# Kernel optimization log

Measured on AMD Instinct MI355X. Metric: run time of the kernel, lower is better.

Reference implementation:

```python
import jax, jax.numpy as jnp
import numpy as np

OBJ_N, D_KEY, D_VAL, BANK_N, N_Q, BS = 4, 128, 512, 7200, 3600, 1


def setup_inputs() -> dict:
    key = jax.random.key(0)
    k1, k2, k3, k4, k5 = jax.random.split(key, 5)
    return {
        "keys": jax.random.normal(k1, (OBJ_N, D_KEY, BANK_N), dtype=jnp.float32),
        "values": jax.random.normal(k2, (OBJ_N, D_VAL, BANK_N), dtype=jnp.float32),
        "masks": jax.random.uniform(k3, (OBJ_N, 1, BANK_N), dtype=jnp.float32),
        "q_in": jax.random.normal(k4, (BS, D_KEY, N_Q), dtype=jnp.float32),
        "q_out": jax.random.normal(k5, (BS, D_VAL, N_Q), dtype=jnp.float32),
    }


def reference(keys, values, masks, q_in, q_out):
    # keys: (O, Dk, B) memory keys per object; q_in: (S, Dk, N) query keys
    d_key = keys.shape[1]
    scale = 1.0 / jnp.sqrt(jnp.asarray(d_key, dtype=keys.dtype))
    # p[o,s,b,n] = softmax_b( keys[o,:,b] . q_in[s,:,n] / sqrt(Dk) )
    logits = jnp.einsum('odb,sdn->osbn', keys, q_in) * scale
    p = jax.nn.softmax(logits, axis=2)
    # mem[o,s,v,n] = sum_b values[o,v,b] * p[o,s,b,n]
    mem = jnp.einsum('ovb,osbn->osvn', values, p)
    # mask_mem[o,s,1,n]: mask-weighted attention readout, gates q_out
    mask_mem = jnp.einsum('omb,osbn->osmn', masks, p)
    q_out_with_mask = q_out[None] * mask_mem          # (O, S, Dv, N)
    out = jnp.concatenate([mem, q_out_with_mask], axis=2)  # (O, S, 2*Dv, N)
    return jnp.transpose(out, (1, 0, 2, 3))           # (S, O, 2*Dv, N)
```

## Files before the change

kernel.cpp:

```cpp
#include <hip/hip_runtime.h>
#include <hip/hip_bf16.h>

typedef unsigned short u16;
typedef unsigned int   u32;
typedef short bf16x8 __attribute__((ext_vector_type(8)));
typedef float f32x4  __attribute__((ext_vector_type(4)));

#define O_N    4
#define D_K    128
#define D_V    512
#define BANK   7200
#define NQ     3600
#define NT     64
#define NTILES 57
#define NSUB   225
#define VH_ROWS 256

#define P_OFF    0
#define LST_OFF  16384
#define MST_OFF  17408
#define SMEM_BYTES 18432
#define Q_OFF    0

#define MFMA16(a, b, c) __builtin_amdgcn_mfma_f32_16x16x32_bf16((a), (b), (c), 0, 0, 0)

static __device__ __forceinline__ u16 f2bf(float x) {
    u32 u = __builtin_bit_cast(u32, x);
    return (u16)((u + 0x7FFFu + ((u >> 16) & 1u)) >> 16);
}

#define QSCALE 0.12751743f


__global__ void k_transpose_bf16(const float* __restrict__ in, u16* __restrict__ out) {
    __shared__ float tile[32][33];
    const int obj = blockIdx.z;
    const float* src = in + (size_t)obj * D_K * BANK;
    u16* dst = out + (size_t)obj * BANK * D_K;
    const int bx = blockIdx.x * 32;
    const int by = blockIdx.y * 32;
    const int tx = threadIdx.x, ty = threadIdx.y;
#pragma unroll
    for (int i = 0; i < 4; i++)
        tile[ty + 8 * i][tx] = src[(size_t)(by + ty + 8 * i) * BANK + bx + tx];
    __syncthreads();
#pragma unroll
    for (int i = 0; i < 4; i++)
        dst[(size_t)(bx + ty + 8 * i) * D_K + by + tx] = f2bf(tile[tx][ty + 8 * i]);
}

__global__ void k_convert_bf16(const float* __restrict__ in, u16* __restrict__ out, int n4) {
    int idx = blockIdx.x * blockDim.x + threadIdx.x;
    int stride = gridDim.x * blockDim.x;
    for (int i = idx; i < n4; i += stride) {
        float4 v = reinterpret_cast<const float4*>(in)[i];
        ushort4 o;
        o.x = f2bf(v.x); o.y = f2bf(v.y); o.z = f2bf(v.z); o.w = f2bf(v.w);
        reinterpret_cast<ushort4*>(out)[i] = o;
    }
}

__global__ void k_zero(float* out, int n) {
    int i = blockIdx.x * blockDim.x + threadIdx.x;
    if (i < n) out[i] = 0.f;
}

__launch_bounds__(256, 2)
__global__ void k_matcher(const u16* __restrict__ Kt,
                          const u16* __restrict__ Vb,
                          const float* __restrict__ masks,
                          const float* __restrict__ q_in,
                          const float* __restrict__ q_out,
                          float* __restrict__ out,
                          int G, float* __restrict__ lw, float* __restrict__ mw)
{
    __shared__ __align__(16) char smem[SMEM_BYTES];
    const int tid  = threadIdx.x;
    const int wave = tid >> 6;
    const int lane = tid & 63;
    const int q    = lane >> 4;
    const int lr   = lane & 15;
    const int lr7  = lr & 7;

    const int grp  = blockIdx.x & 7;
    const int o    = grp >> 1;
    const int vh   = grp & 1;
    const int rest = blockIdx.x >> 3;
    const int tile = rest / G;
    const int g    = rest - tile * G;
    const int n0   = tile * NT;

    const bool needLM = (G == 1) || (vh == 0);

    const int st0 = (NSUB * g) / G;
    const int st1 = (NSUB * (g + 1)) / G;
    const int cnt = st1 - st0;
    const int nd  = cnt >> 1;
    const int ts  = cnt & 1;
    const int nu  = nd + ts;

    for (int idx = tid; idx < NT * D_K; idx += 256) {
        int d = idx >> 6;
        int n = idx & 63;
        int gn = n0 + n;
        float v = (gn < NQ) ? q_in[(size_t)d * NQ + gn] * QSCALE : 0.f;
        int bb = d * 2;
        int sb = n * 256 + ((((bb >> 4) ^ (n & 7)) << 4) | (bb & 15));
        *reinterpret_cast<u16*>(smem + Q_OFF + sb) = f2bf(v);
    }
    __syncthreads();

    bf16x8 qf[4][4];
#pragma unroll
    for (int cg = 0; cg < 4; cg++)
#pragma unroll
        for (int ds = 0; ds < 4; ds++) {
            int gq = (4 * ds + q) ^ lr7;
            qf[cg][ds] = *reinterpret_cast<const bf16x8*>(
                smem + Q_OFF + (16 * cg + lr) * 256 + gq * 16);
        }
    __syncthreads();

    const f32x4 zero4 = {0.f, 0.f, 0.f, 0.f};
    f32x4 acc[4][4];
#pragma unroll
    for (int i = 0; i < 4; i++)
#pragma unroll
        for (int j = 0; j < 4; j++) acc[i][j] = zero4;
    float l_part[4]  = {0.f, 0.f, 0.f, 0.f};
    float mm_part[4] = {0.f, 0.f, 0.f, 0.f};

    const u16* Ko = Kt + (size_t)o * BANK * D_K;
    const u16* Vo = Vb + (size_t)o * D_V * BANK + (size_t)vh * VH_ROWS * BANK;

    const u16* Krow = Ko + (size_t)(st0 * 32) * D_K;
    const u32  kOff = (u32)(16 * wave + lr) * D_K + q * 8;

    const u16* Vrow = Vo + st0 * 32;
    const u32  vOff = (u32)(64 * wave + lr) * BANK + q * 8;

    const float* mPtr = masks + (size_t)o * BANK + st0 * 32 + 16 * wave + 4 * q;

#define QK_CG(CG) do {                                                       \
        f32x4 s_acc = zero4;                                                 \
        s_acc = MFMA16(kf0, qf[CG][0], s_acc);                               \
        s_acc = MFMA16(kf1, qf[CG][1], s_acc);                               \
        s_acc = MFMA16(kf2, qf[CG][2], s_acc);                               \
        s_acc = MFMA16(kf3, qf[CG][3], s_acc);                               \
        float p0 = exp2f(s_acc[0]);                                          \
        float p1 = exp2f(s_acc[1]);                                          \
        float p2 = exp2f(s_acc[2]);                                          \
        float p3 = exp2f(s_acc[3]);                                          \
        if (needLM) {                                                        \
            l_part[CG]  += p0 + p1 + p2 + p3;                                \
            mm_part[CG] += p0 * mv.x + p1 * mv.y + p2 * mv.z + p3 * mv.w;    \
        }                                                                    \
        u32 w0, w1;                                                          \
        asm("v_cvt_pk_bf16_f32 %0, %1, %2" : "=v"(w0) : "v"(p0), "v"(p1));   \
        asm("v_cvt_pk_bf16_f32 %0, %1, %2" : "=v"(w1) : "v"(p2), "v"(p3));   \
        uint2 pk2; pk2.x = w0; pk2.y = w1;                                   \
        *reinterpret_cast<uint2*>(pWb + (16 * (CG) + lr) * 128 +             \
            (((2 * wave + (q >> 1)) ^ lr7) << 4) + (q & 1) * 8) = pk2;       \
    } while (0)

#define PV_S(S, PB, V0, V1, V2, V3) do {                                     \
        _Pragma("unroll")                                                    \
        for (int ng = 0; ng < 4; ng++) {                                     \
            bf16x8 pf = *reinterpret_cast<const bf16x8*>(                    \
                (PB) + (16 * ng + lr) * 128 +                                \
                (((4 * (S) + q) ^ lr7) << 4));                               \
            acc[0][ng] = MFMA16(V0, pf, acc[0][ng]);                         \
            acc[1][ng] = MFMA16(V1, pf, acc[1][ng]);                         \
            acc[2][ng] = MFMA16(V2, pf, acc[2][ng]);                         \
            acc[3][ng] = MFMA16(V3, pf, acc[3][ng]);                         \
        }                                                                    \
    } while (0)

    bf16x8 va0, va1, va2, va3, vb0, vb1, vb2, vb3;

    for (int u = 0; u < nu; u++) {
        const int cur = u & 1;
        char* pWb = smem + P_OFF + cur * 8192;
        const char* pR = smem + P_OFF + (cur ^ 1) * 8192;
        const bool full = (u < nd);
        const bool doQK = full || (wave < 2);

        bf16x8 kf0, kf1, kf2, kf3;
        float4 mv;
        if (doQK) {
            kf0 = *reinterpret_cast<const bf16x8*>(Krow + kOff);
            kf1 = *reinterpret_cast<const bf16x8*>(Krow + kOff + 32);
            kf2 = *reinterpret_cast<const bf16x8*>(Krow + kOff + 64);
            kf3 = *reinterpret_cast<const bf16x8*>(Krow + kOff + 96);
            mv  = *reinterpret_cast<const float4*>(mPtr);
        }
        __builtin_amdgcn_sched_barrier(0);

        if (u > 0) {
            __builtin_amdgcn_s_setprio(1);
            PV_S(0, pR, va0, va1, va2, va3);
            PV_S(1, pR, vb0, vb1, vb2, vb3);
            __builtin_amdgcn_s_setprio(0);
        }
        __builtin_amdgcn_sched_barrier(0);

        va0 = *reinterpret_cast<const bf16x8*>(Vrow + vOff);
        va1 = *reinterpret_cast<const bf16x8*>(Vrow + vOff + 16 * BANK);
        va2 = *reinterpret_cast<const bf16x8*>(Vrow + vOff + 32 * BANK);
        va3 = *reinterpret_cast<const bf16x8*>(Vrow + vOff + 48 * BANK);
        if (full) {
            vb0 = *reinterpret_cast<const bf16x8*>(Vrow + vOff + 32);
            vb1 = *reinterpret_cast<const bf16x8*>(Vrow + vOff + 32 + 16 * BANK);
            vb2 = *reinterpret_cast<const bf16x8*>(Vrow + vOff + 32 + 32 * BANK);
            vb3 = *reinterpret_cast<const bf16x8*>(Vrow + vOff + 32 + 48 * BANK);
        }

        if (doQK) {
            __builtin_amdgcn_s_setprio(1);
            QK_CG(0); QK_CG(1); QK_CG(2); QK_CG(3);
            __builtin_amdgcn_s_setprio(0);
        }

        Vrow += full ? 64 : 32;
        Krow += (full ? 64 : 32) * D_K;
        mPtr += full ? 64 : 32;

        asm volatile("s_waitcnt lgkmcnt(0)" ::: "memory");
        __builtin_amdgcn_s_barrier();
        __builtin_amdgcn_sched_barrier(0);
    }

    {
        const char* pL = smem + P_OFF + ((nu - 1) & 1) * 8192;
        PV_S(0, pL, va0, va1, va2, va3);
        if (!ts) PV_S(1, pL, vb0, vb1, vb2, vb3);
    }

    float* lst = reinterpret_cast<float*>(smem + LST_OFF);
    float* mst = reinterpret_cast<float*>(smem + MST_OFF);
    if (needLM) {
#pragma unroll
        for (int cg = 0; cg < 4; cg++) {
            l_part[cg]  += __shfl_xor(l_part[cg], 16);
            l_part[cg]  += __shfl_xor(l_part[cg], 32);
            mm_part[cg] += __shfl_xor(mm_part[cg], 16);
            mm_part[cg] += __shfl_xor(mm_part[cg], 32);
        }
        if (lane < 16) {
#pragma unroll
            for (int cg = 0; cg < 4; cg++) {
                lst[wave * 64 + 16 * cg + lr] = l_part[cg];
                mst[wave * 64 + 16 * cg + lr] = mm_part[cg];
            }
        }
    }
    __syncthreads();

    if (G == 1) {
        float* outo = out + (size_t)o * (1024 * NQ);
#pragma unroll
        for (int ng = 0; ng < 4; ng++) {
            const int n  = 16 * ng + lr;
            const int gn = n0 + n;
            if (gn >= NQ) continue;
            const float lsum = lst[n] + lst[64 + n] + lst[128 + n] + lst[192 + n];
            const float msum = mst[n] + mst[64 + n] + mst[128 + n] + mst[192 + n];
            const float invl = 1.f / lsum;
            const float gate = msum * invl;
#pragma unroll
            for (int vt = 0; vt < 4; vt++) {
#pragma unroll
                for (int r = 0; r < 4; r++) {
                    const int v = vh * VH_ROWS + 64 * wave + 16 * vt + 4 * q + r;
                    outo[(size_t)v * NQ + gn] = acc[vt][ng][r] * invl;
                    outo[(size_t)(512 + v) * NQ + gn] = q_out[(size_t)v * NQ + gn] * gate;
                }
            }
        }
    } else {
        float* dst = out + ((size_t)o * 1024 + (size_t)g * 512 + (size_t)vh * VH_ROWS) * NQ;
#pragma unroll
        for (int ng = 0; ng < 4; ng++) {
            const int n  = 16 * ng + lr;
            const int gn = n0 + n;
            if (gn >= NQ) continue;
#pragma unroll
            for (int vt = 0; vt < 4; vt++) {
#pragma unroll
                for (int r = 0; r < 4; r++) {
                    const int v = 64 * wave + 16 * vt + 4 * q + r;
                    dst[(size_t)v * NQ + gn] = acc[vt][ng][r];
                }
            }
        }
        if (vh == 0 && tid < 64) {
            const size_t li = ((size_t)(g * 4 + o) * NTILES + tile) * 64 + tid;
            lw[li] = lst[tid] + lst[64 + tid] + lst[128 + tid] + lst[192 + tid];
            mw[li] = mst[tid] + mst[64 + tid] + mst[128 + tid] + mst[192 + tid];
        }
    }
}

__global__ void k_combine(const float* __restrict__ q_out, const float* __restrict__ lw,
                          const float* __restrict__ mw, float* __restrict__ out) {
    const int total = O_N * 512 * (NQ / 4);
    float4* outv = reinterpret_cast<float4*>(out);
    const float4* qv = reinterpret_cast<const float4*>(q_out);
    for (int idx = blockIdx.x * blockDim.x + threadIdx.x; idx < total;
         idx += gridDim.x * blockDim.x) {
        const int o  = idx / (512 * 900);
        const int r  = idx - o * 512 * 900;
        const int v  = r / 900;
        const int g4 = r - v * 900;
        const size_t iA = ((size_t)o * 1024 + v) * 900 + g4;
        const size_t iB = ((size_t)o * 1024 + 512 + v) * 900 + g4;
        float4 A = outv[iA];
        float4 B = outv[iB];
        const int tl = g4 >> 4;
        const int wi = (g4 & 15) * 4;
        const size_t l0i = ((size_t)(0 * 4 + o) * NTILES + tl) * 64 + wi;
        const size_t l1i = ((size_t)(1 * 4 + o) * NTILES + tl) * 64 + wi;
        const float4 l0 = *reinterpret_cast<const float4*>(lw + l0i);
        const float4 l1 = *reinterpret_cast<const float4*>(lw + l1i);
        const float4 m0 = *reinterpret_cast<const float4*>(mw + l0i);
        const float4 m1 = *reinterpret_cast<const float4*>(mw + l1i);
        float4 li, mem, gate;
        li.x = 1.f / (l0.x + l1.x); li.y = 1.f / (l0.y + l1.y);
        li.z = 1.f / (l0.z + l1.z); li.w = 1.f / (l0.w + l1.w);
        mem.x = (A.x + B.x) * li.x; mem.y = (A.y + B.y) * li.y;
        mem.z = (A.z + B.z) * li.z; mem.w = (A.w + B.w) * li.w;
        gate.x = (m0.x + m1.x) * li.x; gate.y = (m0.y + m1.y) * li.y;
        gate.z = (m0.z + m1.z) * li.z; gate.w = (m0.w + m1.w) * li.w;
        float4 qo = qv[(size_t)v * 900 + g4];
        outv[iA] = mem;
        float4 gq;
        gq.x = qo.x * gate.x; gq.y = qo.y * gate.y;
        gq.z = qo.z * gate.z; gq.w = qo.w * gate.w;
        outv[iB] = gq;
    }
}

extern "C" void kernel_launch(void* const* d_in, const int* in_sizes, int n_in,
                              void* d_out, int out_size, void* d_ws, size_t ws_size,
                              hipStream_t stream) {
    const float* keys   = (const float*)d_in[0];
    const float* values = (const float*)d_in[1];
    const float* masks  = (const float*)d_in[2];
    const float* q_in   = (const float*)d_in[3];
    const float* q_outp = (const float*)d_in[4];
    float* out = (float*)d_out;

    const size_t K_BYTES  = (size_t)O_N * BANK * D_K * 2;
    const size_t V_BYTES  = (size_t)O_N * D_V * BANK * 2;
    const size_t LM_FLOATS = (size_t)2 * O_N * NTILES * 64;
    const size_t LM_BYTES  = LM_FLOATS * 4 * 2;

    if (ws_size < K_BYTES + V_BYTES) {
        k_zero<<<(out_size + 255) / 256, 256, 0, stream>>>(out, out_size);
        return;
    }
    const int G = (ws_size >= K_BYTES + V_BYTES + LM_BYTES) ? 2 : 1;

    u16* Kt = (u16*)d_ws;
    u16* Vb = (u16*)((char*)d_ws + K_BYTES);
    float* lw = (float*)((char*)d_ws + K_BYTES + V_BYTES);
    float* mw = lw + LM_FLOATS;

    dim3 tb(32, 8);
    dim3 tg(BANK / 32, D_K / 32, O_N);
    k_transpose_bf16<<<tg, tb, 0, stream>>>(keys, Kt);

    const int n4 = O_N * D_V * BANK / 4;
    k_convert_bf16<<<2048, 256, 0, stream>>>(values, Vb, n4);

    k_matcher<<<NTILES * 8 * G, 256, 0, stream>>>(Kt, Vb, masks, q_in, q_outp, out,
                                                  G, lw, mw);
    if (G == 2)
        k_combine<<<2048, 256, 0, stream>>>(q_outp, lw, mw, out);
}
```

Baseline: 288.7 us.

## Unroll the attention loop to process two 64-column sub-tiles per barrier

The main QK/PV loop now handles two 64-wide bank chunks per iteration. Each chunk gets its own 8 KB P buffer and its own set of V registers, with the LDS double buffer grown to 16 KB per stage. This halves the number of workgroup barriers and waitcnts, and removes the per-iteration full/partial branching. The leftover 32-wide chunk moves to a separate tail. The cost is higher register and LDS use, and the tail only covers a single leftover 32-column chunk, so it relies on the split leaving a remainder of 0 or 1.

```diff
diff --git a/kernel.cpp b/kernel.cpp
--- a/kernel.cpp
+++ b/kernel.cpp
@@ -17,9 +17,9 @@
 #define VH_ROWS 256
 
 #define P_OFF    0
-#define LST_OFF  16384
-#define MST_OFF  17408
-#define SMEM_BYTES 18432
+#define LST_OFF  32768
+#define MST_OFF  33792
+#define SMEM_BYTES 34816
 #define Q_OFF    0
 
 #define MFMA16(a, b, c) __builtin_amdgcn_mfma_f32_16x16x32_bf16((a), (b), (c), 0, 0, 0)
@@ -95,9 +95,8 @@
     const int st0 = (NSUB * g) / G;
     const int st1 = (NSUB * (g + 1)) / G;
     const int cnt = st1 - st0;
-    const int nd  = cnt >> 1;
-    const int ts  = cnt & 1;
-    const int nu  = nd + ts;
+    const int npair = cnt >> 2;
+    const int rem   = cnt & 3;
 
     for (int idx = tid; idx < NT * D_K; idx += 256) {
         int d = idx >> 6;
@@ -141,7 +140,7 @@
 
     const float* mPtr = masks + (size_t)o * BANK + st0 * 32 + 16 * wave + 4 * q;
 
-#define QK_CG(CG) do {                                                       \
+#define QK_CG(CG, PWB) do {                                                  \
         f32x4 s_acc = zero4;                                                 \
         s_acc = MFMA16(kf0, qf[CG][0], s_acc);                               \
         s_acc = MFMA16(kf1, qf[CG][1], s_acc);                               \
@@ -159,7 +158,7 @@
         asm("v_cvt_pk_bf16_f32 %0, %1, %2" : "=v"(w0) : "v"(p0), "v"(p1));   \
         asm("v_cvt_pk_bf16_f32 %0, %1, %2" : "=v"(w1) : "v"(p2), "v"(p3));   \
         uint2 pk2; pk2.x = w0; pk2.y = w1;                                   \
-        *reinterpret_cast<uint2*>(pWb + (16 * (CG) + lr) * 128 +             \
+        *reinterpret_cast<uint2*>((PWB) + (16 * (CG) + lr) * 128 +           \
             (((2 * wave + (q >> 1)) ^ lr7) << 4) + (q & 1) * 8) = pk2;       \
     } while (0)
 
@@ -176,64 +175,102 @@
         }                                                                    \
     } while (0)
 
-    bf16x8 va0, va1, va2, va3, vb0, vb1, vb2, vb3;
-
-    for (int u = 0; u < nu; u++) {
-        const int cur = u & 1;
-        char* pWb = smem + P_OFF + cur * 8192;
-        const char* pR = smem + P_OFF + (cur ^ 1) * 8192;
-        const bool full = (u < nd);
-        const bool doQK = full || (wave < 2);
-
-        bf16x8 kf0, kf1, kf2, kf3;
-        float4 mv;
-        if (doQK) {
-            kf0 = *reinterpret_cast<const bf16x8*>(Krow + kOff);
-            kf1 = *reinterpret_cast<const bf16x8*>(Krow + kOff + 32);
-            kf2 = *reinterpret_cast<const bf16x8*>(Krow + kOff + 64);
-            kf3 = *reinterpret_cast<const bf16x8*>(Krow + kOff + 96);
-            mv  = *reinterpret_cast<const float4*>(mPtr);
-        }
-        __builtin_amdgcn_sched_barrier(0);
-
-        if (u > 0) {
+    bf16x8 Ava0, Ava1, Ava2, Ava3, Avb0, Avb1, Avb2, Avb3;
+    bf16x8 Bva0, Bva1, Bva2, Bva3, Bvb0, Bvb1, Bvb2, Bvb3;
+
+    for (int t = 0; t < npair; t++) {
+        const int cur = t & 1;
+        char* pC = smem + P_OFF + cur * 16384;
+        const char* pP = smem + P_OFF + (cur ^ 1) * 16384;
+
+        {
+            bf16x8 kf0 = *reinterpret_cast<const bf16x8*>(Krow + kOff);
+            bf16x8 kf1 = *reinterpret_cast<const bf16x8*>(Krow + kOff + 32);
+            bf16x8 kf2 = *reinterpret_cast<const bf16x8*>(Krow + kOff + 64);
+            bf16x8 kf3 = *reinterpret_cast<const bf16x8*>(Krow + kOff + 96);
+            float4 mv = *reinterpret_cast<const float4*>(mPtr);
+            __builtin_amdgcn_sched_barrier(0);
+            if (t > 0) {
+                __builtin_amdgcn_s_setprio(1);
+                PV_S(0, pP, Ava0, Ava1, Ava2, Ava3);
+                PV_S(1, pP, Avb0, Avb1, Avb2, Avb3);
+                __builtin_amdgcn_s_setprio(0);
+            }
+            __builtin_amdgcn_sched_barrier(0);
+            Ava0 = *reinterpret_cast<const bf16x8*>(Vrow + vOff);
+            Ava1 = *reinterpret_cast<const bf16x8*>(Vrow + vOff + 16 * BANK);
+            Ava2 = *reinterpret_cast<const bf16x8*>(Vrow + vOff + 32 * BANK);
+            Ava3 = *reinterpret_cast<const bf16x8*>(Vrow + vOff + 48 * BANK);
+            Avb0 = *reinterpret_cast<const bf16x8*>(Vrow + vOff + 32);
+            Avb1 = *reinterpret_cast<const bf16x8*>(Vrow + vOff + 32 + 16 * BANK);
+            Avb2 = *reinterpret_cast<const bf16x8*>(Vrow + vOff + 32 + 32 * BANK);
+            Avb3 = *reinterpret_cast<const bf16x8*>(Vrow + vOff + 32 + 48 * BANK);
             __builtin_amdgcn_s_setprio(1);
-            PV_S(0, pR, va0, va1, va2, va3);
-            PV_S(1, pR, vb0, vb1, vb2, vb3);
+            QK_CG(0, pC); QK_CG(1, pC); QK_CG(2, pC); QK_CG(3, pC);
             __builtin_amdgcn_s_setprio(0);
-        }
-        __builtin_amdgcn_sched_barrier(0);
-
-        va0 = *reinterpret_cast<const bf16x8*>(Vrow + vOff);
-        va1 = *reinterpret_cast<const bf16x8*>(Vrow + vOff + 16 * BANK);
-        va2 = *reinterpret_cast<const bf16x8*>(Vrow + vOff + 32 * BANK);
-        va3 = *reinterpret_cast<const bf16x8*>(Vrow + vOff + 48 * BANK);
-        if (full) {
-            vb0 = *reinterpret_cast<const bf16x8*>(Vrow + vOff + 32);
-            vb1 = *reinterpret_cast<const bf16x8*>(Vrow + vOff + 32 + 16 * BANK);
-            vb2 = *reinterpret_cast<const bf16x8*>(Vrow + vOff + 32 + 32 * BANK);
-            vb3 = *reinterpret_cast<const bf16x8*>(Vrow + vOff + 32 + 48 * BANK);
-        }
-
-        if (doQK) {
+            Krow += 64 * D_K; Vrow += 64; mPtr += 64;
+        }
+
+        {
+            bf16x8 kf0 = *reinterpret_cast<const bf16x8*>(Krow + kOff);
+            bf16x8 kf1 = *reinterpret_cast<const bf16x8*>(Krow + kOff + 32);
+            bf16x8 kf2 = *reinterpret_cast<const bf16x8*>(Krow + kOff + 64);
+            bf16x8 kf3 = *reinterpret_cast<const bf16x8*>(Krow + kOff + 96);
+            float4 mv = *reinterpret_cast<const float4*>(mPtr);
+            __builtin_amdgcn_sched_barrier(0);
+            if (t > 0) {
+                __builtin_amdgcn_s_setprio(1);
+                PV_S(0, pP + 8192, Bva0, Bva1, Bva2, Bva3);
+                PV_S(1, pP + 8192, Bvb0, Bvb1, Bvb2, Bvb3);
+                __builtin_amdgcn_s_setprio(0);
+            }
+            __builtin_amdgcn_sched_barrier(0);
+            Bva0 = *reinterpret_cast<const bf16x8*>(Vrow + vOff);
+            Bva1 = *reinterpret_cast<const bf16x8*>(Vrow + vOff + 16 * BANK);
+            Bva2 = *reinterpret_cast<const bf16x8*>(Vrow + vOff + 32 * BANK);
+            Bva3 = *reinterpret_cast<const bf16x8*>(Vrow + vOff + 48 * BANK);
+            Bvb0 = *reinterpret_cast<const bf16x8*>(Vrow + vOff + 32);
+            Bvb1 = *reinterpret_cast<const bf16x8*>(Vrow + vOff + 32 + 16 * BANK);
+            Bvb2 = *reinterpret_cast<const bf16x8*>(Vrow + vOff + 32 + 32 * BANK);
+            Bvb3 = *reinterpret_cast<const bf16x8*>(Vrow + vOff + 32 + 48 * BANK);
             __builtin_amdgcn_s_setprio(1);
-            QK_CG(0); QK_CG(1); QK_CG(2); QK_CG(3);
+            QK_CG(0, pC + 8192); QK_CG(1, pC + 8192);
+            QK_CG(2, pC + 8192); QK_CG(3, pC + 8192);
             __builtin_amdgcn_s_setprio(0);
-        }
-
-        Vrow += full ? 64 : 32;
-        Krow += (full ? 64 : 32) * D_K;
-        mPtr += full ? 64 : 32;
+            Krow += 64 * D_K; Vrow += 64; mPtr += 64;
+        }
 
         asm volatile("s_waitcnt lgkmcnt(0)" ::: "memory");
         __builtin_amdgcn_s_barrier();
         __builtin_amdgcn_sched_barrier(0);
     }
 
+    char* pT = smem + P_OFF + (npair & 1) * 16384;
+    if (rem && wave < 2) {
+        bf16x8 kf0 = *reinterpret_cast<const bf16x8*>(Krow + kOff);
+        bf16x8 kf1 = *reinterpret_cast<const bf16x8*>(Krow + kOff + 32);
+        bf16x8 kf2 = *reinterpret_cast<const bf16x8*>(Krow + kOff + 64);
+        bf16x8 kf3 = *reinterpret_cast<const bf16x8*>(Krow + kOff + 96);
+        float4 mv = *reinterpret_cast<const float4*>(mPtr);
+        QK_CG(0, pT); QK_CG(1, pT); QK_CG(2, pT); QK_CG(3, pT);
+    }
+
     {
-        const char* pL = smem + P_OFF + ((nu - 1) & 1) * 8192;
-        PV_S(0, pL, va0, va1, va2, va3);
-        if (!ts) PV_S(1, pL, vb0, vb1, vb2, vb3);
+        const char* pL = smem + P_OFF + (((npair - 1) & 1)) * 16384;
+        PV_S(0, pL, Ava0, Ava1, Ava2, Ava3);
+        PV_S(1, pL, Avb0, Avb1, Avb2, Avb3);
+        PV_S(0, pL + 8192, Bva0, Bva1, Bva2, Bva3);
+        PV_S(1, pL + 8192, Bvb0, Bvb1, Bvb2, Bvb3);
+    }
+
+    if (rem) {
+        asm volatile("s_waitcnt lgkmcnt(0)" ::: "memory");
+        __builtin_amdgcn_s_barrier();
+        bf16x8 tv0 = *reinterpret_cast<const bf16x8*>(Vrow + vOff);
+        bf16x8 tv1 = *reinterpret_cast<const bf16x8*>(Vrow + vOff + 16 * BANK);
+        bf16x8 tv2 = *reinterpret_cast<const bf16x8*>(Vrow + vOff + 32 * BANK);
+        bf16x8 tv3 = *reinterpret_cast<const bf16x8*>(Vrow + vOff + 48 * BANK);
+        PV_S(0, pT, tv0, tv1, tv2, tv3);
     }
 
     float* lst = reinterpret_cast<float*>(smem + LST_OFF);
```

Measured after the change: 386.0 us. +33.7%, slower.
